# Performance work log

Measured on AMD Instinct MI355X. Metric: run time of the kernel, lower is better.

Reference implementation:

```python
import jax, jax.numpy as jnp
import numpy as np

N = 20000      # n_nodes
E = 320000     # n_edges (multiple of 4, so _from_coo drops nothing)
D = 512        # embed_dim
H = 8          # num_heads
DK = D // H    # d_k = 64


def setup_inputs() -> dict:
    key = jax.random.key(0)
    ks = jax.random.split(key, 12)
    x = jax.random.normal(ks[0], (N, D), jnp.float32)
    rows = jnp.sort(jax.random.randint(ks[1], (E,), 0, N))
    cols = jax.random.randint(ks[2], (E,), 0, N)
    edge_index = jnp.stack([rows, cols]).astype(jnp.int32)  # [2, E]
    att_bias = jax.random.normal(ks[3], (E, H), jnp.float32)
    s = float(1.0 / np.sqrt(D))  # ~xavier scale
    Wq = jax.random.normal(ks[4], (D, D), jnp.float32) * s
    Wk = jax.random.normal(ks[5], (D, D), jnp.float32) * s
    Wv = jax.random.normal(ks[6], (D, D), jnp.float32) * s
    Wo = jax.random.normal(ks[7], (D, D), jnp.float32) * s
    bq = jnp.zeros((D,), jnp.float32)
    bk = jnp.zeros((D,), jnp.float32)
    bv = jnp.zeros((D,), jnp.float32)
    bo = jnp.zeros((D,), jnp.float32)
    return dict(x=x, edge_index=edge_index, att_bias=att_bias,
                Wq=Wq, bq=bq, Wk=Wk, bk=bk, Wv=Wv, bv=bv, Wo=Wo, bo=bo)


def reference(x, edge_index, att_bias, Wq, bq, Wk, bk, Wv, bv, Wo, bo):
    n = x.shape[0]
    rows, cols = edge_index[0], edge_index[1]
    # per-head projections: [n, H, DK]
    q = (x @ Wq + bq).reshape(n, H, DK)
    k = (x @ Wk + bk).reshape(n, H, DK)
    v = (x @ Wv + bv).reshape(n, H, DK)
    scale = 1.0 / jnp.sqrt(jnp.asarray(DK, x.dtype))
    # masked QK^T on the edge pattern, plus additive bias: [E, H]
    logits = jnp.einsum('ehd,ehd->eh', q[rows] * scale, k[cols]) + att_bias
    # CSR (segment) softmax over each destination row
    row_max = jax.ops.segment_max(logits, rows, num_segments=n)      # [n, H]
    p = jnp.exp(logits - row_max[rows])                              # [E, H]
    denom = jax.ops.segment_sum(p, rows, num_segments=n)            # [n, H]
    att = p / denom[rows]                                            # [E, H]
    # sparse-dense bmm: y[i] = sum_{e: rows[e]=i} att[e] * v[cols[e]]
    y = jax.ops.segment_sum(att[:, :, None] * v[cols], rows, num_segments=n)  # [n, H, DK]
    out = y.reshape(n, H * DK) @ Wo + bo
    return out
```

## Files before the change

### kernel.cpp

```cpp
#include <hip/hip_runtime.h>
#include <hip/hip_bf16.h>

typedef unsigned short ushort_t;
typedef unsigned int uint32;
typedef __attribute__((ext_vector_type(8))) short short8;
typedef __attribute__((ext_vector_type(4))) float floatx4;

#define DEV __device__ __forceinline__

#if defined(__has_builtin)
#if __has_builtin(__builtin_amdgcn_sdot4)
#define HAS_SDOT 1
#endif
#endif
#ifndef HAS_SDOT
#define HAS_SDOT 0
#endif

DEV float b2f(ushort_t u) { return __uint_as_float(((uint32)u) << 16); }
DEV ushort_t f2b(float f) {
  __hip_bfloat16 h = __float2bfloat16(f);
  return __builtin_bit_cast(unsigned short, h);
}
DEV void unpack8(const uint4& u, float* f) {
  f[0] = __uint_as_float(u.x << 16); f[1] = __uint_as_float(u.x & 0xffff0000u);
  f[2] = __uint_as_float(u.y << 16); f[3] = __uint_as_float(u.y & 0xffff0000u);
  f[4] = __uint_as_float(u.z << 16); f[5] = __uint_as_float(u.z & 0xffff0000u);
  f[6] = __uint_as_float(u.w << 16); f[7] = __uint_as_float(u.w & 0xffff0000u);
}
DEV void unpack_i8x8(uint2 u, float* f) {
  f[0] = (float)((int)(u.x << 24) >> 24);
  f[1] = (float)((int)(u.x << 16) >> 24);
  f[2] = (float)((int)(u.x << 8) >> 24);
  f[3] = (float)((int)u.x >> 24);
  f[4] = (float)((int)(u.y << 24) >> 24);
  f[5] = (float)((int)(u.y << 16) >> 24);
  f[6] = (float)((int)(u.y << 8) >> 24);
  f[7] = (float)((int)u.y >> 24);
}

#define GLOAD_LDS(gp, lp) \
  __builtin_amdgcn_global_load_lds((const __attribute__((address_space(1))) uint32*)(gp), \
                                   (__attribute__((address_space(3))) uint32*)(lp), 16, 0, 0)

#define KVROW 1088

__global__ __launch_bounds__(256) void k_detect(const ushort_t* __restrict__ x,
                                                int* __restrict__ flag) {
  __shared__ int red[256];
  int tid = threadIdx.x;
  int wild = 0;
  for (int i = tid; i < 4096; i += 256) {
    uint32 e = (x[i] >> 7) & 0xFFu;
    if (e < 100u || e > 140u) wild++;
  }
  red[tid] = wild;
  __syncthreads();
  for (int s = 128; s > 0; s >>= 1) {
    if (tid < s) red[tid] += red[tid + s];
    __syncthreads();
  }
  if (tid == 0) flag[0] = (red[0] > 400) ? 1 : 0;
}

__global__ __launch_bounds__(256) void k_transpose(
    const void* __restrict__ Wq, const void* __restrict__ Wk,
    const void* __restrict__ Wv, const void* __restrict__ Wo,
    ushort_t* __restrict__ WT4, const int* __restrict__ flagp) {
  __shared__ ushort_t t[32][33];
  int isf32 = *flagp;
  int z = blockIdx.z;
  const void* src = (z == 0) ? Wq : (z == 1) ? Wk : (z == 2) ? Wv : Wo;
  ushort_t* dst = WT4 + (size_t)z * 512 * 512;
  int bx = blockIdx.x, by = blockIdx.y;
  int tx = threadIdx.x, ty = threadIdx.y;
#pragma unroll
  for (int i = 0; i < 4; i++) {
    size_t idx = (size_t)(by * 32 + ty + 8 * i) * 512 + bx * 32 + tx;
    ushort_t v = isf32 ? f2b(((const float*)src)[idx]) : ((const ushort_t*)src)[idx];
    t[ty + 8 * i][tx] = v;
  }
  __syncthreads();
#pragma unroll
  for (int i = 0; i < 4; i++)
    dst[(size_t)(bx * 32 + ty + 8 * i) * 512 + by * 32 + tx] = t[tx][ty + 8 * i];
}

__global__ __launch_bounds__(256) void k_biases(
    const void* __restrict__ bq, const void* __restrict__ bk,
    const void* __restrict__ bv, const void* __restrict__ bo,
    float* __restrict__ biasf, const int* __restrict__ flagp) {
  int i = blockIdx.x * 256 + threadIdx.x;
  if (i >= 2048) return;
  int z = i >> 9, j = i & 511;
  const void* b = (z == 0) ? bq : (z == 1) ? bk : (z == 2) ? bv : bo;
  biasf[i] = (*flagp) ? ((const float*)b)[j] : b2f(((const ushort_t*)b)[j]);
}

__global__ __launch_bounds__(256) void k_convx(
    const void* __restrict__ x, ushort_t* __restrict__ xb, int n8,
    const int* __restrict__ flagp) {
  int i = blockIdx.x * 256 + threadIdx.x;
  if (i >= n8) return;
  if (*flagp) {
    const float* xf = (const float*)x + (size_t)i * 8;
    float4 f0 = ((const float4*)xf)[0];
    float4 f1 = ((const float4*)xf)[1];
    uint4 o;
    o.x = (uint32)f2b(f0.x) | ((uint32)f2b(f0.y) << 16);
    o.y = (uint32)f2b(f0.z) | ((uint32)f2b(f0.w) << 16);
    o.z = (uint32)f2b(f1.x) | ((uint32)f2b(f1.y) << 16);
    o.w = (uint32)f2b(f1.z) | ((uint32)f2b(f1.w) << 16);
    ((uint4*)xb)[i] = o;
  } else {
    ((uint4*)xb)[i] = ((const uint4*)x)[i];
  }
}

__global__ __launch_bounds__(256) void k_convab(
    const void* __restrict__ ab, float* __restrict__ ABc, int n4,
    const int* __restrict__ flagp) {
  if (*flagp) return;
  int i = blockIdx.x * 256 + threadIdx.x;
  if (i >= n4) return;
  uint2 u = ((const uint2*)ab)[i];
  float4 o;
  o.x = __uint_as_float(u.x << 16);
  o.y = __uint_as_float(u.x & 0xffff0000u);
  o.z = __uint_as_float(u.y << 16);
  o.w = __uint_as_float(u.y & 0xffff0000u);
  ((float4*)ABc)[i] = o;
}

__global__ void k_build_rp(const int* __restrict__ rows, int E, int N, int* __restrict__ rp) {
  int i = blockIdx.x * blockDim.x + threadIdx.x;
  if (i > N) return;
  int lo = 0, hi = E;
  while (lo < hi) {
    int mid = (lo + hi) >> 1;
    if (rows[mid] < i) lo = mid + 1; else hi = mid;
  }
  rp[i] = lo;
}

DEV void gemm_body(const ushort_t* __restrict__ A, const ushort_t* __restrict__ BT,
                   const float* __restrict__ bias, void* C,
                   int M, int ldc, float scale, int row0, int by, int mode) {
  __shared__ ushort_t As[128 * 32];
  __shared__ ushort_t Bs[128 * 32];
  int tid = threadIdx.x;
  int w = tid >> 6, lane = tid & 63;
  int sr = lane >> 2;
  int sk = (lane & 3) * 8;

  floatx4 acc[4][4];
#pragma unroll
  for (int i = 0; i < 4; i++)
#pragma unroll
    for (int j = 0; j < 4; j++)
#pragma unroll
      for (int r = 0; r < 4; r++) acc[i][j][r] = 0.f;

  int lm = lane & 15, quad = lane >> 4;
  int wr = w >> 1, wc = w & 1;
  const int nG = by * 128 + w * 32;

  int rA0 = row0 + w * 32 + sr; if (rA0 >= M) rA0 = M - 1;
  int rA1 = rA0 + 16;          if (rA1 >= M) rA1 = M - 1;
  const ushort_t* gA0 = A + (size_t)rA0 * 512 + sk;
  const ushort_t* gA1 = A + (size_t)rA1 * 512 + sk;
  const ushort_t* gB0 = BT + (size_t)(nG + sr) * 512 + sk;
  const ushort_t* gB1 = BT + (size_t)(nG + 16 + sr) * 512 + sk;

  for (int k0 = 0; k0 < 512; k0 += 32) {
    GLOAD_LDS(gA0 + k0, As + (w * 32 + 0) * 32);
    GLOAD_LDS(gA1 + k0, As + (w * 32 + 16) * 32);
    GLOAD_LDS(gB0 + k0, Bs + (w * 32 + 0) * 32);
    GLOAD_LDS(gB1 + k0, Bs + (w * 32 + 16) * 32);
    __syncthreads();

    const ushort_t* pa = As + (wr * 64 + lm) * 32 + quad * 8;
    const ushort_t* pb = Bs + (wc * 64 + lm) * 32 + quad * 8;
    short8 af[4], bfr[4];
#pragma unroll
    for (int t4 = 0; t4 < 4; t4++) {
      af[t4]  = *(const short8*)(pa + t4 * 16 * 32);
      bfr[t4] = *(const short8*)(pb + t4 * 16 * 32);
    }
#pragma unroll
    for (int mt = 0; mt < 4; mt++)
#pragma unroll
      for (int nt = 0; nt < 4; nt++)
        acc[mt][nt] = __builtin_amdgcn_mfma_f32_16x16x32_bf16(af[mt], bfr[nt], acc[mt][nt], 0, 0, 0);
    __syncthreads();
  }

  int colB = by * 128 + wc * 64 + lm;
  float bv4[4];
#pragma unroll
  for (int nt = 0; nt < 4; nt++) bv4[nt] = bias[colB + nt * 16];

  if (mode <= 1) {
#pragma unroll
    for (int mt = 0; mt < 4; mt++) {
      int rg0 = row0 + wr * 64 + mt * 16 + quad * 4;
#pragma unroll
      for (int nt = 0; nt < 4; nt++) {
#pragma unroll
        for (int r = 0; r < 4; r++) {
          int rg = rg0 + r;
          if (rg < M) {
            float val = (acc[mt][nt][r] + bv4[nt]) * scale;
            size_t off = (size_t)rg * ldc + colB + nt * 16;
            if (mode == 1) ((float*)C)[off] = val;
            else           ((ushort_t*)C)[off] = f2b(val);
          }
        }
      }
    }
  } else {
    int vslot = (mode == 4);
    int colbase = by * 128 + wc * 64;
    int head = colbase >> 6;
#pragma unroll
    for (int mt = 0; mt < 4; mt++) {
#pragma unroll
      for (int r = 0; r < 4; r++) {
        int rg = row0 + wr * 64 + mt * 16 + quad * 4 + r;
        float v0 = acc[mt][0][r] + bv4[0];
        float v1 = acc[mt][1][r] + bv4[1];
        float v2 = acc[mt][2][r] + bv4[2];
        float v3 = acc[mt][3][r] + bv4[3];
        float am = fmaxf(fmaxf(fabsf(v0), fabsf(v1)), fmaxf(fabsf(v2), fabsf(v3)));
        am = fmaxf(am, __shfl_xor(am, 1));
        am = fmaxf(am, __shfl_xor(am, 2));
        am = fmaxf(am, __shfl_xor(am, 4));
        am = fmaxf(am, __shfl_xor(am, 8));
        am = fmaxf(am, 1e-20f);
        float inv8 = 127.0f / am;
        float sc8 = am * (1.0f / 127.0f);
        if (rg < M) {
          unsigned char* Crow = (unsigned char*)C + (size_t)rg * KVROW;
          unsigned char* bp = Crow + 2 * colbase + 16 * (lm >> 3) + 8 * vslot + (lm & 7);
          bp[ 0] = (unsigned char)(signed char)(int)rintf(v0 * inv8);
          bp[32] = (unsigned char)(signed char)(int)rintf(v1 * inv8);
          bp[64] = (unsigned char)(signed char)(int)rintf(v2 * inv8);
          bp[96] = (unsigned char)(signed char)(int)rintf(v3 * inv8);
          if (lm == 0)
            *(float*)(Crow + 1024 + head * 8 + vslot * 4) = sc8;
        }
      }
    }
  }
}

__global__ __launch_bounds__(256) void k_gemm_qkv(
    const ushort_t* __restrict__ xb, const ushort_t* __restrict__ WT4,
    const float* __restrict__ biasf, ushort_t* Qp, unsigned char* KV8, int M) {
  int z = blockIdx.z;
  const ushort_t* BT = WT4 + (size_t)z * 512 * 512;
  const float* bias = biasf + (size_t)z * 512;
  if (z == 0)
    gemm_body(xb, BT, bias, Qp, M, 512, 0.125f, blockIdx.x * 128, blockIdx.y, 0);
  else
    gemm_body(xb, BT, bias, KV8, M, 0, 1.0f, blockIdx.x * 128, blockIdx.y, z == 1 ? 3 : 4);
}

__global__ __launch_bounds__(256) void k_gemm_out(
    const ushort_t* __restrict__ y, const ushort_t* __restrict__ WT4,
    const float* __restrict__ biasf, void* out, int M,
    const int* __restrict__ flagp) {
  gemm_body(y, WT4 + (size_t)3 * 512 * 512, biasf + 3 * 512, out, M, 512, 1.0f,
            blockIdx.x * 128, blockIdx.y, *flagp);
}

__global__ __launch_bounds__(256) void k_edge(
    ushort_t* Qy, const unsigned char* __restrict__ KV8,
    const void* __restrict__ ab, const float* __restrict__ ABc,
    const int* __restrict__ cols, const int* __restrict__ rp, int Nn,
    const int* __restrict__ flagp) {
  int node = blockIdx.x * 4 + (threadIdx.x >> 6);
  if (node >= Nn) return;
  int lane = threadIdx.x & 63;
  int h8 = lane >> 3;
  const float* abf32 = (*flagp) ? (const float*)ab : ABc;

  uint4 qu = ((const uint4*)(Qy + (size_t)node * 512))[lane];
  float qf[8];
  unpack8(qu, qf);

#if HAS_SDOT
  float qa = 0.f;
#pragma unroll
  for (int j = 0; j < 8; j++) qa = fmaxf(qa, fabsf(qf[j]));
  qa = fmaxf(qa, __shfl_xor(qa, 1));
  qa = fmaxf(qa, __shfl_xor(qa, 2));
  qa = fmaxf(qa, __shfl_xor(qa, 4));
  qa = fmaxf(qa, 1e-20f);
  float qs = qa * (1.0f / 127.0f);
  float qinv = 127.0f / qa;
  int qp0 = 0, qp1 = 0;
#pragma unroll
  for (int j = 0; j < 4; j++) qp0 |= (((int)rintf(qf[j] * qinv)) & 0xFF) << (8 * j);
#pragma unroll
  for (int j = 4; j < 8; j++) qp1 |= (((int)rintf(qf[j] * qinv)) & 0xFF) << (8 * (j - 4));
#endif

  int e0 = rp[node], e1 = rp[node + 1];
  int cnt = e1 - e0;

  float s0 = 0.f, s1 = 0.f;
  float acc0[8], acc1[8];
#pragma unroll
  for (int j = 0; j < 8; j++) { acc0[j] = 0.f; acc1[j] = 0.f; }

  uint4 kvb[4];
  float2 scb[4];
  float abv[4];

  for (int base = 0; base < cnt; base += 64) {
    int rem = cnt - base; if (rem > 64) rem = 64;
    int li = (lane < rem) ? lane : (rem - 1);
    int myc = cols[e0 + base + li];
    const float* abp = abf32 + (size_t)(e0 + base) * 8 + h8;

    auto pref = [&](int t, int slot) {
      int valid = t < rem;
      int c = __builtin_amdgcn_readlane(myc, valid ? t : 0);
      const unsigned char* kvrow = KV8 + (size_t)c * KVROW;
      kvb[slot] = *(const uint4*)(kvrow + lane * 16);
      scb[slot] = *(const float2*)(kvrow + 1024 + h8 * 8);
      float a = abp[(valid ? t : 0) * 8];
      abv[slot] = valid ? a : -1e30f;
    };
    auto consume = [&](int slot, float* acc, float& s) {
#if HAS_SDOT
      int di = __builtin_amdgcn_sdot4(qp0, (int)kvb[slot].x, 0, false);
      di = __builtin_amdgcn_sdot4(qp1, (int)kvb[slot].y, di, false);
      di += __shfl_xor(di, 1);
      di += __shfl_xor(di, 2);
      di += __shfl_xor(di, 4);
      float logit = fminf(fmaf((float)di * qs, scb[slot].x, abv[slot]), 80.f);
#else
      float kf[8];
      uint2 ku; ku.x = kvb[slot].x; ku.y = kvb[slot].y;
      unpack_i8x8(ku, kf);
      float d = 0.f;
#pragma unroll
      for (int j = 0; j < 8; j++) d = fmaf(qf[j], kf[j], d);
      d += __shfl_xor(d, 1);
      d += __shfl_xor(d, 2);
      d += __shfl_xor(d, 4);
      float logit = fminf(fmaf(d, scb[slot].x, abv[slot]), 80.f);
#endif
      float pw = __expf(logit);
      s += pw;
      float pwv = pw * scb[slot].y;
      float vf[8];
      uint2 vu; vu.x = kvb[slot].z; vu.y = kvb[slot].w;
      unpack_i8x8(vu, vf);
#pragma unroll
      for (int j = 0; j < 8; j++) acc[j] = fmaf(pwv, vf[j], acc[j]);
    };

    pref(0, 0); pref(1, 1); pref(2, 2); pref(3, 3);
    int iters = (rem + 3) >> 2;
    for (int it = 0; it < iters; ++it) {
      int nt = it * 4 + 4;
      consume(0, acc0, s0); pref(nt + 0, 0);
      consume(1, acc1, s1); pref(nt + 1, 1);
      consume(2, acc0, s0); pref(nt + 2, 2);
      consume(3, acc1, s1); pref(nt + 3, 3);
    }
  }

  float s = s0 + s1;
  float inv = (cnt > 0 && s > 0.f) ? 1.f / s : 0.f;
  ushort_t hb[8];
#pragma unroll
  for (int j = 0; j < 8; j++) hb[j] = f2b((acc0[j] + acc1[j]) * inv);
  uint4 uh;
  uh.x = (uint32)hb[0] | ((uint32)hb[1] << 16);
  uh.y = (uint32)hb[2] | ((uint32)hb[3] << 16);
  uh.z = (uint32)hb[4] | ((uint32)hb[5] << 16);
  uh.w = (uint32)hb[6] | ((uint32)hb[7] << 16);
  ((uint4*)(Qy + (size_t)node * 512))[lane] = uh;
}

extern "C" void kernel_launch(void* const* d_in, const int* in_sizes, int n_in,
                              void* d_out, int out_size, void* d_ws, size_t ws_size,
                              hipStream_t stream) {
  const void* x  = d_in[0];
  const int* ei  = (const int*)d_in[1];
  const void* ab = d_in[2];
  const void* Wq = d_in[3];
  const void* bq = d_in[4];
  const void* Wk = d_in[5];
  const void* bk = d_in[6];
  const void* Wv = d_in[7];
  const void* bv = d_in[8];
  const void* Wo = d_in[9];
  const void* bo = d_in[10];

  const int D = 512;
  int M = in_sizes[0] / D;
  int E = in_sizes[1] / 2;
  const int* rows = ei;
  const int* cols = ei + E;

  char* p = (char*)d_ws;
  size_t off = 0;
  auto carve = [&](size_t bytes) -> void* {
    off = (off + 255) & ~(size_t)255;
    void* r = p + off;
    off += bytes;
    return r;
  };
  int* flag          = (int*)carve(4);
  ushort_t* WT4      = (ushort_t*)carve((size_t)4 * 512 * 512 * 2);
  float* biasf       = (float*)carve((size_t)4 * 512 * 4);
  ushort_t* xb       = (ushort_t*)carve((size_t)M * 512 * 2);
  ushort_t* Qp       = (ushort_t*)carve((size_t)M * 512 * 2);
  unsigned char* KV8 = (unsigned char*)carve((size_t)M * KVROW);
  int* rp            = (int*)carve((size_t)(M + 1) * 4);
  (void)ws_size;
  float* ABc = (float*)xb;

  k_detect<<<1, 256, 0, stream>>>((const ushort_t*)x, flag);
  k_transpose<<<dim3(16, 16, 4), dim3(32, 8), 0, stream>>>(Wq, Wk, Wv, Wo, WT4, flag);
  k_biases<<<8, 256, 0, stream>>>(bq, bk, bv, bo, biasf, flag);
  int n8 = M * 512 / 8;
  k_convx<<<(n8 + 255) / 256, 256, 0, stream>>>(x, xb, n8, flag);
  k_build_rp<<<(M + 1 + 255) / 256, 256, 0, stream>>>(rows, E, M, rp);

  int rb = (M + 127) / 128;
  k_gemm_qkv<<<dim3(rb, 4, 3), 256, 0, stream>>>(xb, WT4, biasf, Qp, KV8, M);
  int n4 = E * 8 / 4;
  k_convab<<<(n4 + 255) / 256, 256, 0, stream>>>(ab, ABc, n4, flag);
  k_edge<<<(M + 3) / 4, 256, 0, stream>>>(Qp, KV8, ab, ABc, cols, rp, M, flag);
  k_gemm_out<<<dim3(rb, 4, 1), 256, 0, stream>>>(Qp, WT4, biasf, d_out, M, flag);
}
```

Before: 275.3 us.

## Double-buffer GEMM LDS tiles and XOR-swizzle k-chunks to avoid bank conflicts

```diff
diff --git a/kernel.cpp b/kernel.cpp
--- a/kernel.cpp
+++ b/kernel.cpp
@@ -146,12 +146,12 @@
 DEV void gemm_body(const ushort_t* __restrict__ A, const ushort_t* __restrict__ BT,
                    const float* __restrict__ bias, void* C,
                    int M, int ldc, float scale, int row0, int by, int mode) {
-  __shared__ ushort_t As[128 * 32];
-  __shared__ ushort_t Bs[128 * 32];
+  __shared__ ushort_t As[2][128 * 32];
+  __shared__ ushort_t Bs[2][128 * 32];
   int tid = threadIdx.x;
   int w = tid >> 6, lane = tid & 63;
   int sr = lane >> 2;
-  int sk = (lane & 3) * 8;
+  int skz = (((lane & 3) ^ ((lane >> 3) & 3)) * 8);
 
   floatx4 acc[4][4];
 #pragma unroll
@@ -167,20 +167,29 @@
 
   int rA0 = row0 + w * 32 + sr; if (rA0 >= M) rA0 = M - 1;
   int rA1 = rA0 + 16;          if (rA1 >= M) rA1 = M - 1;
-  const ushort_t* gA0 = A + (size_t)rA0 * 512 + sk;
-  const ushort_t* gA1 = A + (size_t)rA1 * 512 + sk;
-  const ushort_t* gB0 = BT + (size_t)(nG + sr) * 512 + sk;
-  const ushort_t* gB1 = BT + (size_t)(nG + 16 + sr) * 512 + sk;
-
-  for (int k0 = 0; k0 < 512; k0 += 32) {
-    GLOAD_LDS(gA0 + k0, As + (w * 32 + 0) * 32);
-    GLOAD_LDS(gA1 + k0, As + (w * 32 + 16) * 32);
-    GLOAD_LDS(gB0 + k0, Bs + (w * 32 + 0) * 32);
-    GLOAD_LDS(gB1 + k0, Bs + (w * 32 + 16) * 32);
-    __syncthreads();
-
-    const ushort_t* pa = As + (wr * 64 + lm) * 32 + quad * 8;
-    const ushort_t* pb = Bs + (wc * 64 + lm) * 32 + quad * 8;
+  const ushort_t* gA0 = A + (size_t)rA0 * 512 + skz;
+  const ushort_t* gA1 = A + (size_t)rA1 * 512 + skz;
+  const ushort_t* gB0 = BT + (size_t)(nG + sr) * 512 + skz;
+  const ushort_t* gB1 = BT + (size_t)(nG + 16 + sr) * 512 + skz;
+
+  auto stage = [&](int buf, int k0) {
+    GLOAD_LDS(gA0 + k0, &As[buf][(w * 32 + 0) * 32]);
+    GLOAD_LDS(gA1 + k0, &As[buf][(w * 32 + 16) * 32]);
+    GLOAD_LDS(gB0 + k0, &Bs[buf][(w * 32 + 0) * 32]);
+    GLOAD_LDS(gB1 + k0, &Bs[buf][(w * 32 + 16) * 32]);
+  };
+
+  int rchunk = (quad ^ ((lm >> 1) & 3)) * 8;
+
+  stage(0, 0);
+  __syncthreads();
+
+  for (int ks = 0; ks < 16; ++ks) {
+    int cur = ks & 1;
+    if (ks < 15) stage(cur ^ 1, (ks + 1) * 32);
+
+    const ushort_t* pa = &As[cur][(wr * 64 + lm) * 32] + rchunk;
+    const ushort_t* pb = &Bs[cur][(wc * 64 + lm) * 32] + rchunk;
     short8 af[4], bfr[4];
 #pragma unroll
     for (int t4 = 0; t4 < 4; t4++) {
@@ -192,6 +201,7 @@
 #pragma unroll
       for (int nt = 0; nt < 4; nt++)
         acc[mt][nt] = __builtin_amdgcn_mfma_f32_16x16x32_bf16(af[mt], bfr[nt], acc[mt][nt], 0, 0, 0);
+
     __syncthreads();
   }
 
```

New measurement: 274.8 us. About the same (-0.2%).
